# Performance work log

Hardware: AMD Instinct MI355X
Metric: run time of the kernel (lower is better)

Reference implementation:

```python
import jax, jax.numpy as jnp
import numpy as np

V, T_BLOCK, E, H, L = 65, 256, 384, 6, 10
HS = E // H  # 64


def _ln(x, scale, bias, eps=1e-5):
    mu = jnp.mean(x, axis=-1, keepdims=True)
    var = jnp.mean(jnp.square(x - mu), axis=-1, keepdims=True)
    return (x - mu) * jax.lax.rsqrt(var + eps) * scale + bias


def setup_inputs() -> dict:
    key = jax.random.key(0)
    ks = jax.random.split(key, 20)
    B, T = 64, 256
    s = 0.02
    return {
        "encoding": jax.random.randint(ks[0], (B, T), 0, V),
        "tok_emb": jax.random.normal(ks[1], (V, E), jnp.float32) * s,
        "pos_emb": jax.random.normal(ks[2], (T_BLOCK, E), jnp.float32) * s,
        "Wq": jax.random.normal(ks[3], (L, H, E, HS), jnp.float32) * s,
        "Wk": jax.random.normal(ks[4], (L, H, E, HS), jnp.float32) * s,
        "Wv": jax.random.normal(ks[5], (L, H, E, HS), jnp.float32) * s,
        "Wo": jax.random.normal(ks[6], (L, E, E), jnp.float32) * s,
        "bo": jnp.zeros((L, E), jnp.float32),
        "W1": jax.random.normal(ks[7], (L, E, 4 * E), jnp.float32) * s,
        "b1": jnp.zeros((L, 4 * E), jnp.float32),
        "W2": jax.random.normal(ks[8], (L, 4 * E, E), jnp.float32) * s,
        "b2": jnp.zeros((L, E), jnp.float32),
        "ln1_s": jnp.ones((L, E), jnp.float32),
        "ln1_b": jnp.zeros((L, E), jnp.float32),
        "ln2_s": jnp.ones((L, E), jnp.float32),
        "ln2_b": jnp.zeros((L, E), jnp.float32),
        "lnf_s": jnp.ones((E,), jnp.float32),
        "lnf_b": jnp.zeros((E,), jnp.float32),
        "Wout": jax.random.normal(ks[9], (E, V), jnp.float32) * s,
        "bout": jnp.zeros((V,), jnp.float32),
    }


def reference(encoding, tok_emb, pos_emb, Wq, Wk, Wv, Wo, bo, W1, b1, W2, b2,
              ln1_s, ln1_b, ln2_s, ln2_b, lnf_s, lnf_b, Wout, bout):
    B, T = encoding.shape
    x = tok_emb[encoding] + pos_emb[:T]  # [B,T,E]
    causal = jnp.tril(jnp.ones((T, T), bool))
    scale = jnp.asarray(E, x.dtype) ** -0.5  # NOTE: original scales by embeddingSize, not headSize
    for l in range(L):
        h = _ln(x, ln1_s[l], ln1_b[l])
        q = jnp.einsum('bte,hed->bhtd', h, Wq[l])
        k = jnp.einsum('bte,hed->bhtd', h, Wk[l])
        v = jnp.einsum('bte,hed->bhtd', h, Wv[l])
        scores = jnp.einsum('bhtd,bhsd->bhts', q, k) * scale
        scores = jnp.where(causal, scores, -jnp.inf)
        w = jax.nn.softmax(scores, axis=-1)  # dropout inactive (eval)
        attn = jnp.einsum('bhts,bhsd->bhtd', w, v)  # [B,H,T,HS]
        attn = attn.transpose(0, 2, 1, 3).reshape(B, T, E)  # concat heads
        x = x + attn @ Wo[l] + bo[l]
        h2 = _ln(x, ln2_s[l], ln2_b[l])
        x = x + jax.nn.relu(h2 @ W1[l] + b1[l]) @ W2[l] + b2[l]
    x = _ln(x, lnf_s, lnf_b)
    logits = x @ Wout + bout  # [B,T,V]
    return logits
```

## Files before the change

kernel.cpp:

```cpp
#include <hip/hip_runtime.h>

typedef __bf16 bf16;
typedef __bf16 bf16x4 __attribute__((ext_vector_type(4)));
typedef __bf16 bf16x8 __attribute__((ext_vector_type(8)));
typedef float floatx4 __attribute__((ext_vector_type(4)));

#define NB   64
#define NT   256
#define NE   384
#define NH   6
#define NHS  64
#define NL   10
#define NTOK (NB*NT)
#define NFF  1536
#define NQKV 1152
#define NV   65
#define NVP  128

#define ATTN_SCALE 0.051031036307982884f

__device__ __forceinline__ void glds16(const bf16* g, bf16* l)
{
    __builtin_amdgcn_global_load_lds(
        (const __attribute__((address_space(1))) void*)g,
        (__attribute__((address_space(3))) void*)l, 16, 0, 0);
}

template<int K, int N>
__global__ __launch_bounds__(256) void pack_mat_t(const float* __restrict__ src, bf16* __restrict__ dst)
{
    __shared__ float tile[64][65];
    const int n0 = blockIdx.x * 64, k0 = blockIdx.y * 64, l = blockIdx.z;
    const int tid = threadIdx.x;
    const float* sp = src + (size_t)l * K * N;
#pragma unroll
    for (int it = 0; it < 4; ++it) {
        int kl = (tid >> 4) + it * 16;
        int nl = (tid & 15) * 4;
        float4 v = *(const float4*)(sp + (size_t)(k0 + kl) * N + n0 + nl);
        tile[kl][nl] = v.x; tile[kl][nl + 1] = v.y; tile[kl][nl + 2] = v.z; tile[kl][nl + 3] = v.w;
    }
    __syncthreads();
#pragma unroll
    for (int it = 0; it < 2; ++it) {
        int chunk = it * 256 + tid;
        int nl = chunk >> 3, kc = chunk & 7;
        bf16x8 o;
#pragma unroll
        for (int j = 0; j < 8; ++j) o[j] = (bf16)tile[kc * 8 + j][nl];
        *(bf16x8*)(dst + ((size_t)l * N + n0 + nl) * K + k0 + kc * 8) = o;
    }
}

__global__ __launch_bounds__(256) void pack_qkv_t(const float* __restrict__ Wq, const float* __restrict__ Wk,
                                                  const float* __restrict__ Wv, bf16* __restrict__ dst)
{
    __shared__ float tile[64][65];
    const int n0 = blockIdx.x * 64, k0 = blockIdx.y * 64, l = blockIdx.z;
    const int tid = threadIdx.x;
    const float* src; int hh;
    if (n0 < 384)      { src = Wq; hh = n0 >> 6; }
    else if (n0 < 768) { src = Wk; hh = (n0 - 384) >> 6; }
    else               { src = Wv; hh = (n0 - 768) >> 6; }
    const float* sp = src + ((size_t)l * NH + hh) * NE * NHS;
#pragma unroll
    for (int it = 0; it < 4; ++it) {
        int kl = (tid >> 4) + it * 16;
        int dl = (tid & 15) * 4;
        float4 v = *(const float4*)(sp + (size_t)(k0 + kl) * NHS + dl);
        tile[kl][dl] = v.x; tile[kl][dl + 1] = v.y; tile[kl][dl + 2] = v.z; tile[kl][dl + 3] = v.w;
    }
    __syncthreads();
#pragma unroll
    for (int it = 0; it < 2; ++it) {
        int chunk = it * 256 + tid;
        int nl = chunk >> 3, kc = chunk & 7;
        bf16x8 o;
#pragma unroll
        for (int j = 0; j < 8; ++j) o[j] = (bf16)tile[kc * 8 + j][nl];
        *(bf16x8*)(dst + ((size_t)l * NQKV + n0 + nl) * NE + k0 + kc * 8) = o;
    }
}

__global__ void pack_wout_kernel(const float* __restrict__ Wout, const float* __restrict__ bout,
                                 bf16* __restrict__ dst, float* __restrict__ bias)
{
    int i = blockIdx.x * 256 + threadIdx.x;
    if (i >= NVP * NE) return;
    int k = i % NE, n = i / NE;
    dst[i] = (n < NV) ? (bf16)Wout[(size_t)k * NV + n] : (bf16)0.f;
    if (i < NVP) bias[i] = (i < NV) ? bout[i] : 0.f;
}

__global__ void embed_kernel(const int* __restrict__ enc, const float* __restrict__ tok,
                             const float* __restrict__ pos, bf16* __restrict__ x)
{
    int i = blockIdx.x * 256 + threadIdx.x;
    if (i >= NTOK * 96) return;
    int row = i / 96, e4 = i % 96;
    int t = row & (NT - 1);
    const float4* tp = (const float4*)(tok + (size_t)enc[row] * NE);
    const float4* pp = (const float4*)(pos + (size_t)t * NE);
    float4 a = tp[e4], p = pp[e4];
    bf16x4 r;
    r[0] = (bf16)(a.x + p.x); r[1] = (bf16)(a.y + p.y);
    r[2] = (bf16)(a.z + p.z); r[3] = (bf16)(a.w + p.w);
    *(bf16x4*)(x + (size_t)row * NE + e4 * 4) = r;
}

__global__ __launch_bounds__(256) void ln_kernel(const bf16* __restrict__ xin,
                                                 const float* __restrict__ gam,
                                                 const float* __restrict__ bet,
                                                 bf16* __restrict__ out)
{
    int wave = threadIdx.x >> 6, lane = threadIdx.x & 63;
    size_t row = (size_t)blockIdx.x * 4 + wave;
    const bf16x4* xr = (const bf16x4*)(xin + row * NE);
    bf16x4 c0 = xr[lane];
    bf16x4 c1 = (lane < 32) ? xr[64 + lane] : (bf16x4)(bf16)0.f;
    float v[8]; float sum = 0.f;
#pragma unroll
    for (int j = 0; j < 4; ++j) { v[j] = (float)c0[j]; sum += v[j]; }
#pragma unroll
    for (int j = 0; j < 4; ++j) { v[4 + j] = (float)c1[j]; sum += v[4 + j]; }
#pragma unroll
    for (int o = 1; o < 64; o <<= 1) sum += __shfl_xor(sum, o);
    float mu = sum * (1.f / NE);
    float var = 0.f;
#pragma unroll
    for (int j = 0; j < 4; ++j) { float d = v[j] - mu; var += d * d; }
    if (lane < 32) {
#pragma unroll
        for (int j = 0; j < 4; ++j) { float d = v[4 + j] - mu; var += d * d; }
    }
#pragma unroll
    for (int o = 1; o < 64; o <<= 1) var += __shfl_xor(var, o);
    float rs = rsqrtf(var * (1.f / NE) + 1e-5f);
    bf16x4* orow = (bf16x4*)(out + row * NE);
    {
        float4 g = ((const float4*)gam)[lane], bb = ((const float4*)bet)[lane];
        bf16x4 o4;
        o4[0] = (bf16)((v[0] - mu) * rs * g.x + bb.x);
        o4[1] = (bf16)((v[1] - mu) * rs * g.y + bb.y);
        o4[2] = (bf16)((v[2] - mu) * rs * g.z + bb.z);
        o4[3] = (bf16)((v[3] - mu) * rs * g.w + bb.w);
        orow[lane] = o4;
    }
    if (lane < 32) {
        float4 g = ((const float4*)gam)[64 + lane], bb = ((const float4*)bet)[64 + lane];
        bf16x4 o4;
        o4[0] = (bf16)((v[4] - mu) * rs * g.x + bb.x);
        o4[1] = (bf16)((v[5] - mu) * rs * g.y + bb.y);
        o4[2] = (bf16)((v[6] - mu) * rs * g.z + bb.z);
        o4[3] = (bf16)((v[7] - mu) * rs * g.w + bb.w);
        orow[64 + lane] = o4;
    }
}

template<int MT, bool BIAS, bool RELU, bool RESID, bool OUTBF16, bool VSPLIT>
__global__ __launch_bounds__(256, 4)
void gemm_kernel(const bf16* __restrict__ A, const bf16* __restrict__ Bt,
                 const float* __restrict__ bias, const bf16* __restrict__ resid,
                 void* __restrict__ outp, bf16* __restrict__ vt,
                 int M, int K, int out_stride, int n_store)
{
    constexpr int MI = MT / 32;
    __shared__ bf16 As[MT * 64];
    __shared__ bf16 Bs[128 * 64];
    const int tid  = threadIdx.x;
    const int wave = tid >> 6;
    const int lane = tid & 63;
    const int quad = lane >> 4;
    const int l16  = lane & 15;
    const int lrow = lane >> 3;
    const int scol = ((lane & 7) ^ lrow) * 8;
    const int m0 = blockIdx.x * MT;
    const int n0 = blockIdx.y * 128;
    const int wm = (wave >> 1) * (MT / 2);
    const int wn = (wave & 1) * 64;

    floatx4 acc[MI][4];
#pragma unroll
    for (int i = 0; i < MI; ++i)
#pragma unroll
        for (int j = 0; j < 4; ++j) acc[i][j] = (floatx4)0.f;

    const bf16* Ag = A  + (size_t)m0 * K;
    const bf16* Bg = Bt + (size_t)n0 * K;

    for (int k0 = 0; k0 < K; k0 += 64) {
#pragma unroll
        for (int it = 0; it < MT / 32; ++it) {
            int r0 = wave * (MT / 4) + it * 8;
            glds16(Ag + (size_t)(r0 + lrow) * K + k0 + scol, &As[r0 * 64]);
        }
#pragma unroll
        for (int it = 0; it < 4; ++it) {
            int r0 = wave * 32 + it * 8;
            glds16(Bg + (size_t)(r0 + lrow) * K + k0 + scol, &Bs[r0 * 64]);
        }
        __syncthreads();
#pragma unroll
        for (int ko = 0; ko < 2; ++ko) {
            bf16x8 af[MI], bfr[4];
#pragma unroll
            for (int mi = 0; mi < MI; ++mi) {
                int r = wm + mi * 16 + l16;
                int c = ((ko * 4 + quad) ^ (r & 7)) * 8;
                af[mi] = *(const bf16x8*)(&As[r * 64 + c]);
            }
#pragma unroll
            for (int ni = 0; ni < 4; ++ni) {
                int r = wn + ni * 16 + l16;
                int c = ((ko * 4 + quad) ^ (r & 7)) * 8;
                bfr[ni] = *(const bf16x8*)(&Bs[r * 64 + c]);
            }
#pragma unroll
            for (int mi = 0; mi < MI; ++mi)
#pragma unroll
                for (int ni = 0; ni < 4; ++ni)
                    acc[mi][ni] = __builtin_amdgcn_mfma_f32_16x16x32_bf16(af[mi], bfr[ni], acc[mi][ni], 0, 0, 0);
        }
        __syncthreads();
    }

#pragma unroll
    for (int mi = 0; mi < MI; ++mi) {
#pragma unroll
        for (int ni = 0; ni < 4; ++ni) {
            int n = n0 + wn + ni * 16 + l16;
            if (VSPLIT && n >= 768) {
                int nn = n - 768;
                int hh = nn >> 6, d = nn & 63;
                int mb = m0 + wm + mi * 16 + quad * 4;
                int bb = mb >> 8, tt = mb & 255;
                bf16x4 pv;
#pragma unroll
                for (int r = 0; r < 4; ++r) pv[r] = (bf16)acc[mi][ni][r];
                *(bf16x4*)(vt + ((size_t)(bb * NH + hh) * NHS + d) * NT + tt) = pv;
                continue;
            }
            float bv = 0.f;
            if (BIAS) bv = bias[n];
#pragma unroll
            for (int r = 0; r < 4; ++r) {
                int m = m0 + wm + mi * 16 + quad * 4 + r;
                float vv = acc[mi][ni][r] + bv;
                if (RELU) vv = fmaxf(vv, 0.f);
                if (n < n_store) {
                    size_t oi = (size_t)m * out_stride + n;
                    if (RESID) vv += (float)resid[oi];
                    if (OUTBF16) ((bf16*)outp)[oi] = (bf16)vv;
                    else         ((float*)outp)[oi] = vv;
                }
            }
        }
    }
}

__global__ __launch_bounds__(256, 3)
void attn_flash_kernel(const bf16* __restrict__ qkv, const bf16* __restrict__ vt,
                       bf16* __restrict__ outp)
{
    __shared__ bf16 Qs[128 * 64];
    __shared__ bf16 Ks[64 * 64];
    __shared__ bf16 Vs[64 * 64];
    __shared__ bf16 Ps[128 * 72];
    const int m0 = blockIdx.x * 128;
    const int z  = blockIdx.y;
    const int b = z / NH, hh = z % NH;
    const int tid = threadIdx.x;
    const int wave = tid >> 6, lane = tid & 63;
    const int quad = lane >> 4, l16 = lane & 15;
    const int lrow = lane >> 3;
    const int scol = ((lane & 7) ^ lrow) * 8;
    const int wm = wave * 32;
    const size_t qbase = (size_t)b * NT * NQKV + hh * NHS;
    const bf16* Vg = vt + (size_t)z * NHS * NT;

#pragma unroll
    for (int it = 0; it < 4; ++it) {
        int r0 = wave * 32 + it * 8;
        glds16(qkv + qbase + (size_t)(m0 + r0 + lrow) * NQKV + scol, &Qs[r0 * 64]);
    }

    floatx4 acc_o[2][4];
    float   psum[2][4];
#pragma unroll
    for (int mi = 0; mi < 2; ++mi) {
#pragma unroll
        for (int ni = 0; ni < 4; ++ni) acc_o[mi][ni] = (floatx4)0.f;
#pragma unroll
        for (int rr = 0; rr < 4; ++rr) psum[mi][rr] = 0.f;
    }

    const int n_ch = (m0 >> 6) + 2;
    for (int ch = 0; ch < n_ch; ++ch) {
        const int s0 = ch * 64;
        {
            int r0 = wave * 16;
            glds16(qkv + qbase + 384 + (size_t)(s0 + r0 + lrow) * NQKV + scol, &Ks[r0 * 64]);
            glds16(qkv + qbase + 384 + (size_t)(s0 + r0 + 8 + lrow) * NQKV + scol, &Ks[(r0 + 8) * 64]);
            glds16(Vg + (size_t)(r0 + lrow) * NT + s0 + scol, &Vs[r0 * 64]);
            glds16(Vg + (size_t)(r0 + 8 + lrow) * NT + s0 + scol, &Vs[(r0 + 8) * 64]);
        }
        __syncthreads();

        floatx4 accs[2][4];
#pragma unroll
        for (int mi = 0; mi < 2; ++mi)
#pragma unroll
            for (int ni = 0; ni < 4; ++ni) accs[mi][ni] = (floatx4)0.f;
#pragma unroll
        for (int ko = 0; ko < 2; ++ko) {
            bf16x8 af[2], bfr[4];
#pragma unroll
            for (int mi = 0; mi < 2; ++mi) {
                int r = wm + mi * 16 + l16;
                af[mi] = *(const bf16x8*)(&Qs[r * 64 + ((ko * 4 + quad) ^ (r & 7)) * 8]);
            }
#pragma unroll
            for (int ni = 0; ni < 4; ++ni) {
                int r = ni * 16 + l16;
                bfr[ni] = *(const bf16x8*)(&Ks[r * 64 + ((ko * 4 + quad) ^ (r & 7)) * 8]);
            }
#pragma unroll
            for (int mi = 0; mi < 2; ++mi)
#pragma unroll
                for (int ni = 0; ni < 4; ++ni)
                    accs[mi][ni] = __builtin_amdgcn_mfma_f32_16x16x32_bf16(af[mi], bfr[ni], accs[mi][ni], 0, 0, 0);
        }

#pragma unroll
        for (int mi = 0; mi < 2; ++mi) {
#pragma unroll
            for (int rr = 0; rr < 4; ++rr) {
                int t = m0 + wm + mi * 16 + quad * 4 + rr;
                float ps = 0.f;
#pragma unroll
                for (int ni = 0; ni < 4; ++ni) {
                    int s = s0 + ni * 16 + l16;
                    float p = (s <= t) ? __expf(accs[mi][ni][rr] * ATTN_SCALE) : 0.f;
                    ps += p;
                    Ps[(wm + mi * 16 + quad * 4 + rr) * 72 + ni * 16 + l16] = (bf16)p;
                }
                psum[mi][rr] += ps;
            }
        }

#pragma unroll
        for (int ko = 0; ko < 2; ++ko) {
            bf16x8 af[2], bfr[4];
#pragma unroll
            for (int mi = 0; mi < 2; ++mi)
                af[mi] = *(const bf16x8*)(&Ps[(wm + mi * 16 + l16) * 72 + ko * 32 + quad * 8]);
#pragma unroll
            for (int ni = 0; ni < 4; ++ni) {
                int r = ni * 16 + l16;
                bfr[ni] = *(const bf16x8*)(&Vs[r * 64 + ((ko * 4 + quad) ^ (r & 7)) * 8]);
            }
#pragma unroll
            for (int mi = 0; mi < 2; ++mi)
#pragma unroll
                for (int ni = 0; ni < 4; ++ni)
                    acc_o[mi][ni] = __builtin_amdgcn_mfma_f32_16x16x32_bf16(af[mi], bfr[ni], acc_o[mi][ni], 0, 0, 0);
        }
        __syncthreads();
    }

#pragma unroll
    for (int mi = 0; mi < 2; ++mi) {
#pragma unroll
        for (int rr = 0; rr < 4; ++rr) {
            float s = psum[mi][rr];
            s += __shfl_xor(s, 1); s += __shfl_xor(s, 2);
            s += __shfl_xor(s, 4); s += __shfl_xor(s, 8);
            psum[mi][rr] = 1.f / s;
        }
    }
#pragma unroll
    for (int mi = 0; mi < 2; ++mi) {
#pragma unroll
        for (int ni = 0; ni < 4; ++ni) {
            int e = hh * NHS + ni * 16 + l16;
#pragma unroll
            for (int rr = 0; rr < 4; ++rr) {
                int m = m0 + wm + mi * 16 + quad * 4 + rr;
                outp[((size_t)b * NT + m) * NE + e] = (bf16)(acc_o[mi][ni][rr] * psum[mi][rr]);
            }
        }
    }
}

extern "C" void kernel_launch(void* const* d_in, const int* in_sizes, int n_in,
                              void* d_out, int out_size, void* d_ws, size_t ws_size,
                              hipStream_t stream)
{
    const int*   enc  = (const int*)d_in[0];
    const float* tok  = (const float*)d_in[1];
    const float* pos  = (const float*)d_in[2];
    const float* Wq   = (const float*)d_in[3];
    const float* Wk   = (const float*)d_in[4];
    const float* Wv   = (const float*)d_in[5];
    const float* Wo   = (const float*)d_in[6];
    const float* bo   = (const float*)d_in[7];
    const float* W1   = (const float*)d_in[8];
    const float* b1   = (const float*)d_in[9];
    const float* W2   = (const float*)d_in[10];
    const float* b2   = (const float*)d_in[11];
    const float* ln1s = (const float*)d_in[12];
    const float* ln1b = (const float*)d_in[13];
    const float* ln2s = (const float*)d_in[14];
    const float* ln2b = (const float*)d_in[15];
    const float* lnfs = (const float*)d_in[16];
    const float* lnfb = (const float*)d_in[17];
    const float* Wout = (const float*)d_in[18];
    const float* bout = (const float*)d_in[19];

    char* ws = (char*)d_ws;
    bf16*  x      = (bf16*)(ws + 0);
    bf16*  h      = (bf16*)(ws + 12582912);
    bf16*  qkvu   = (bf16*)(ws + 25165824);
    bf16*  attn   = (bf16*)(ws + 75497472);
    bf16*  wqkv   = (bf16*)(ws + 88080384);
    bf16*  wo     = (bf16*)(ws + 96927744);
    bf16*  w1     = (bf16*)(ws + 99876864);
    bf16*  w2     = (bf16*)(ws + 111673344);
    bf16*  wop    = (bf16*)(ws + 123469824);
    float* bop    = (float*)(ws + 123568128);
    bf16*  vt     = (bf16*)(ws + 123568640);

    pack_qkv_t<<<dim3(18, 6, NL), 256, 0, stream>>>(Wq, Wk, Wv, wqkv);
    pack_mat_t<384, 384><<<dim3(6, 6, NL), 256, 0, stream>>>(Wo, wo);
    pack_mat_t<384, 1536><<<dim3(24, 6, NL), 256, 0, stream>>>(W1, w1);
    pack_mat_t<1536, 384><<<dim3(6, 24, NL), 256, 0, stream>>>(W2, w2);
    pack_wout_kernel<<<192, 256, 0, stream>>>(Wout, bout, wop, bop);
    embed_kernel<<<6144, 256, 0, stream>>>(enc, tok, pos, x);

    for (int l = 0; l < NL; ++l) {
        ln_kernel<<<4096, 256, 0, stream>>>(x, ln1s + l * NE, ln1b + l * NE, h);
        gemm_kernel<128, false, false, false, true, true><<<dim3(128, 9), 256, 0, stream>>>(
            h, wqkv + (size_t)l * NQKV * NE, nullptr, nullptr, qkvu, vt, NTOK, NE, NQKV, NQKV);
        attn_flash_kernel<<<dim3(2, NB * NH), 256, 0, stream>>>(qkvu, vt, attn);
        gemm_kernel<64, true, false, true, true, false><<<dim3(256, 3), 256, 0, stream>>>(
            attn, wo + (size_t)l * NE * NE, bo + l * NE, x, x, nullptr, NTOK, NE, NE, NE);
        ln_kernel<<<4096, 256, 0, stream>>>(x, ln2s + l * NE, ln2b + l * NE, h);
        gemm_kernel<128, true, true, false, true, false><<<dim3(128, 12), 256, 0, stream>>>(
            h, w1 + (size_t)l * NFF * NE, b1 + l * NFF, nullptr, qkvu, nullptr, NTOK, NE, NFF, NFF);
        gemm_kernel<64, true, false, true, true, false><<<dim3(256, 3), 256, 0, stream>>>(
            qkvu, w2 + (size_t)l * NE * NFF, b2 + l * NE, x, x, nullptr, NTOK, NFF, NE, NE);
    }
    ln_kernel<<<4096, 256, 0, stream>>>(x, lnfs, lnfb, h);
    gemm_kernel<64, true, false, false, false, false><<<dim3(256, 1), 256, 0, stream>>>(
        h, wop, bop, nullptr, d_out, nullptr, NTOK, NE, NV, NV);
}
```

Before: 1.417 ms.

## Fuse LayerNorm into residual GEMM epilogues and embedding kernel

New measurement: 1.620 ms. 14.3% more time.

```diff
diff --git a/kernel.cpp b/kernel.cpp
--- a/kernel.cpp
+++ b/kernel.cpp
@@ -92,37 +92,29 @@
     if (i < NVP) bias[i] = (i < NV) ? bout[i] : 0.f;
 }
 
-__global__ void embed_kernel(const int* __restrict__ enc, const float* __restrict__ tok,
-                             const float* __restrict__ pos, bf16* __restrict__ x)
-{
-    int i = blockIdx.x * 256 + threadIdx.x;
-    if (i >= NTOK * 96) return;
-    int row = i / 96, e4 = i % 96;
-    int t = row & (NT - 1);
+__global__ __launch_bounds__(256) void embed_ln_kernel(const int* __restrict__ enc,
+                                                       const float* __restrict__ tok,
+                                                       const float* __restrict__ pos,
+                                                       const float* __restrict__ gam,
+                                                       const float* __restrict__ bet,
+                                                       bf16* __restrict__ x, bf16* __restrict__ h)
+{
+    int wave = threadIdx.x >> 6, lane = threadIdx.x & 63;
+    size_t row = (size_t)blockIdx.x * 4 + wave;
+    int t = (int)(row & (NT - 1));
     const float4* tp = (const float4*)(tok + (size_t)enc[row] * NE);
     const float4* pp = (const float4*)(pos + (size_t)t * NE);
-    float4 a = tp[e4], p = pp[e4];
-    bf16x4 r;
-    r[0] = (bf16)(a.x + p.x); r[1] = (bf16)(a.y + p.y);
-    r[2] = (bf16)(a.z + p.z); r[3] = (bf16)(a.w + p.w);
-    *(bf16x4*)(x + (size_t)row * NE + e4 * 4) = r;
-}
-
-__global__ __launch_bounds__(256) void ln_kernel(const bf16* __restrict__ xin,
-                                                 const float* __restrict__ gam,
-                                                 const float* __restrict__ bet,
-                                                 bf16* __restrict__ out)
-{
-    int wave = threadIdx.x >> 6, lane = threadIdx.x & 63;
-    size_t row = (size_t)blockIdx.x * 4 + wave;
-    const bf16x4* xr = (const bf16x4*)(xin + row * NE);
-    bf16x4 c0 = xr[lane];
-    bf16x4 c1 = (lane < 32) ? xr[64 + lane] : (bf16x4)(bf16)0.f;
     float v[8]; float sum = 0.f;
-#pragma unroll
-    for (int j = 0; j < 4; ++j) { v[j] = (float)c0[j]; sum += v[j]; }
-#pragma unroll
-    for (int j = 0; j < 4; ++j) { v[4 + j] = (float)c1[j]; sum += v[4 + j]; }
+    {
+        float4 a = tp[lane], p = pp[lane];
+        v[0] = a.x + p.x; v[1] = a.y + p.y; v[2] = a.z + p.z; v[3] = a.w + p.w;
+        sum = v[0] + v[1] + v[2] + v[3];
+    }
+    if (lane < 32) {
+        float4 a = tp[64 + lane], p = pp[64 + lane];
+        v[4] = a.x + p.x; v[5] = a.y + p.y; v[6] = a.z + p.z; v[7] = a.w + p.w;
+        sum += v[4] + v[5] + v[6] + v[7];
+    } else { v[4] = v[5] = v[6] = v[7] = 0.f; }
 #pragma unroll
     for (int o = 1; o < 64; o <<= 1) sum += __shfl_xor(sum, o);
     float mu = sum * (1.f / NE);
@@ -136,24 +128,27 @@
 #pragma unroll
     for (int o = 1; o < 64; o <<= 1) var += __shfl_xor(var, o);
     float rs = rsqrtf(var * (1.f / NE) + 1e-5f);
-    bf16x4* orow = (bf16x4*)(out + row * NE);
+    bf16x4* xrow = (bf16x4*)(x + row * NE);
+    bf16x4* hrow = (bf16x4*)(h + row * NE);
     {
         float4 g = ((const float4*)gam)[lane], bb = ((const float4*)bet)[lane];
-        bf16x4 o4;
-        o4[0] = (bf16)((v[0] - mu) * rs * g.x + bb.x);
-        o4[1] = (bf16)((v[1] - mu) * rs * g.y + bb.y);
-        o4[2] = (bf16)((v[2] - mu) * rs * g.z + bb.z);
-        o4[3] = (bf16)((v[3] - mu) * rs * g.w + bb.w);
-        orow[lane] = o4;
+        bf16x4 xo, ho;
+        xo[0] = (bf16)v[0]; xo[1] = (bf16)v[1]; xo[2] = (bf16)v[2]; xo[3] = (bf16)v[3];
+        ho[0] = (bf16)((v[0] - mu) * rs * g.x + bb.x);
+        ho[1] = (bf16)((v[1] - mu) * rs * g.y + bb.y);
+        ho[2] = (bf16)((v[2] - mu) * rs * g.z + bb.z);
+        ho[3] = (bf16)((v[3] - mu) * rs * g.w + bb.w);
+        xrow[lane] = xo; hrow[lane] = ho;
     }
     if (lane < 32) {
         float4 g = ((const float4*)gam)[64 + lane], bb = ((const float4*)bet)[64 + lane];
-        bf16x4 o4;
-        o4[0] = (bf16)((v[4] - mu) * rs * g.x + bb.x);
-        o4[1] = (bf16)((v[5] - mu) * rs * g.y + bb.y);
-        o4[2] = (bf16)((v[6] - mu) * rs * g.z + bb.z);
-        o4[3] = (bf16)((v[7] - mu) * rs * g.w + bb.w);
-        orow[64 + lane] = o4;
+        bf16x4 xo, ho;
+        xo[0] = (bf16)v[4]; xo[1] = (bf16)v[5]; xo[2] = (bf16)v[6]; xo[3] = (bf16)v[7];
+        ho[0] = (bf16)((v[4] - mu) * rs * g.x + bb.x);
+        ho[1] = (bf16)((v[5] - mu) * rs * g.y + bb.y);
+        ho[2] = (bf16)((v[6] - mu) * rs * g.z + bb.z);
+        ho[3] = (bf16)((v[7] - mu) * rs * g.w + bb.w);
+        xrow[64 + lane] = xo; hrow[64 + lane] = ho;
     }
 }
 
@@ -253,6 +248,112 @@
                     if (OUTBF16) ((bf16*)outp)[oi] = (bf16)vv;
                     else         ((float*)outp)[oi] = vv;
                 }
+            }
+        }
+    }
+}
+
+__global__ __launch_bounds__(256, 2)
+void gemm_resid_ln_kernel(const bf16* __restrict__ A, const bf16* __restrict__ Bt,
+                          const float* __restrict__ bias,
+                          bf16* __restrict__ x, bf16* __restrict__ hout,
+                          const float* __restrict__ gam, const float* __restrict__ bet,
+                          int K)
+{
+    __shared__ bf16 As[64 * 64];
+    __shared__ bf16 Bs[384 * 64];
+    __shared__ float ssum[4][64], ssq[4][64];
+    const int tid  = threadIdx.x;
+    const int wave = tid >> 6;
+    const int lane = tid & 63;
+    const int quad = lane >> 4;
+    const int l16  = lane & 15;
+    const int lrow = lane >> 3;
+    const int scol = ((lane & 7) ^ lrow) * 8;
+    const int m0 = blockIdx.x * 64;
+    const int wn = wave * 96;
+
+    floatx4 acc[4][6];
+#pragma unroll
+    for (int i = 0; i < 4; ++i)
+#pragma unroll
+        for (int j = 0; j < 6; ++j) acc[i][j] = (floatx4)0.f;
+
+    const bf16* Ag = A + (size_t)m0 * K;
+
+    for (int k0 = 0; k0 < K; k0 += 64) {
+        glds16(Ag + (size_t)(wave * 16 + lrow) * K + k0 + scol, &As[(wave * 16) * 64]);
+        glds16(Ag + (size_t)(wave * 16 + 8 + lrow) * K + k0 + scol, &As[(wave * 16 + 8) * 64]);
+#pragma unroll
+        for (int it = 0; it < 12; ++it) {
+            int r0 = wave * 96 + it * 8;
+            glds16(Bt + (size_t)(r0 + lrow) * K + k0 + scol, &Bs[r0 * 64]);
+        }
+        __syncthreads();
+#pragma unroll
+        for (int ko = 0; ko < 2; ++ko) {
+            bf16x8 af[4], bfr[6];
+#pragma unroll
+            for (int mi = 0; mi < 4; ++mi) {
+                int r = mi * 16 + l16;
+                af[mi] = *(const bf16x8*)(&As[r * 64 + ((ko * 4 + quad) ^ (r & 7)) * 8]);
+            }
+#pragma unroll
+            for (int ni = 0; ni < 6; ++ni) {
+                int r = wn + ni * 16 + l16;
+                bfr[ni] = *(const bf16x8*)(&Bs[r * 64 + ((ko * 4 + quad) ^ (r & 7)) * 8]);
+            }
+#pragma unroll
+            for (int mi = 0; mi < 4; ++mi)
+#pragma unroll
+                for (int ni = 0; ni < 6; ++ni)
+                    acc[mi][ni] = __builtin_amdgcn_mfma_f32_16x16x32_bf16(af[mi], bfr[ni], acc[mi][ni], 0, 0, 0);
+        }
+        __syncthreads();
+    }
+
+    float bv[6], gv[6], bb[6];
+#pragma unroll
+    for (int ni = 0; ni < 6; ++ni) {
+        int n = wn + ni * 16 + l16;
+        bv[ni] = bias[n]; gv[ni] = gam[n]; bb[ni] = bet[n];
+    }
+#pragma unroll
+    for (int mi = 0; mi < 4; ++mi) {
+#pragma unroll
+        for (int rr = 0; rr < 4; ++rr) {
+            int rl = mi * 16 + quad * 4 + rr;
+            bf16* xrow = x + (size_t)(m0 + rl) * NE;
+            float s = 0.f, q = 0.f;
+#pragma unroll
+            for (int ni = 0; ni < 6; ++ni) {
+                int n = wn + ni * 16 + l16;
+                float vv = acc[mi][ni][rr] + bv[ni] + (float)xrow[n];
+                acc[mi][ni][rr] = vv;
+                xrow[n] = (bf16)vv;
+                s += vv; q += vv * vv;
+            }
+            s += __shfl_xor(s, 1); s += __shfl_xor(s, 2); s += __shfl_xor(s, 4); s += __shfl_xor(s, 8);
+            q += __shfl_xor(q, 1); q += __shfl_xor(q, 2); q += __shfl_xor(q, 4); q += __shfl_xor(q, 8);
+            if (l16 == 0) { ssum[wave][rl] = s; ssq[wave][rl] = q; }
+        }
+    }
+    __syncthreads();
+#pragma unroll
+    for (int mi = 0; mi < 4; ++mi) {
+#pragma unroll
+        for (int rr = 0; rr < 4; ++rr) {
+            int rl = mi * 16 + quad * 4 + rr;
+            float sum = ssum[0][rl] + ssum[1][rl] + ssum[2][rl] + ssum[3][rl];
+            float sq  = ssq[0][rl]  + ssq[1][rl]  + ssq[2][rl]  + ssq[3][rl];
+            float mu = sum * (1.f / NE);
+            float var = sq * (1.f / NE) - mu * mu;
+            float rs = rsqrtf(var + 1e-5f);
+            bf16* hrow = hout + (size_t)(m0 + rl) * NE;
+#pragma unroll
+            for (int ni = 0; ni < 6; ++ni) {
+                int n = wn + ni * 16 + l16;
+                hrow[n] = (bf16)((acc[mi][ni][rr] - mu) * rs * gv[ni] + bb[ni]);
             }
         }
     }
@@ -435,22 +536,22 @@
     pack_mat_t<384, 1536><<<dim3(24, 6, NL), 256, 0, stream>>>(W1, w1);
     pack_mat_t<1536, 384><<<dim3(6, 24, NL), 256, 0, stream>>>(W2, w2);
     pack_wout_kernel<<<192, 256, 0, stream>>>(Wout, bout, wop, bop);
-    embed_kernel<<<6144, 256, 0, stream>>>(enc, tok, pos, x);
+    embed_ln_kernel<<<4096, 256, 0, stream>>>(enc, tok, pos, ln1s, ln1b, x, h);
 
     for (int l = 0; l < NL; ++l) {
-        ln_kernel<<<4096, 256, 0, stream>>>(x, ln1s + l * NE, ln1b + l * NE, h);
         gemm_kernel<128, false, false, false, true, true><<<dim3(128, 9), 256, 0, stream>>>(
             h, wqkv + (size_t)l * NQKV * NE, nullptr, nullptr, qkvu, vt, NTOK, NE, NQKV, NQKV);
         attn_flash_kernel<<<dim3(2, NB * NH), 256, 0, stream>>>(qkvu, vt, attn);
-        gemm_kernel<64, true, false, true, true, false><<<dim3(256, 3), 256, 0, stream>>>(
-            attn, wo + (size_t)l * NE * NE, bo + l * NE, x, x, nullptr, NTOK, NE, NE, NE);
-        ln_kernel<<<4096, 256, 0, stream>>>(x, ln2s + l * NE, ln2b + l * NE, h);
+        gemm_resid_ln_kernel<<<256, 256, 0, stream>>>(
+            attn, wo + (size_t)l * NE * NE, bo + l * NE, x, h,
+            ln2s + l * NE, ln2b + l * NE, NE);
         gemm_kernel<128, true, true, false, true, false><<<dim3(128, 12), 256, 0, stream>>>(
             h, w1 + (size_t)l * NFF * NE, b1 + l * NFF, nullptr, qkvu, nullptr, NTOK, NE, NFF, NFF);
-        gemm_kernel<64, true, false, true, true, false><<<dim3(256, 3), 256, 0, stream>>>(
-            qkvu, w2 + (size_t)l * NE * NFF, b2 + l * NE, x, x, nullptr, NTOK, NFF, NE, NE);
-    }
-    ln_kernel<<<4096, 256, 0, stream>>>(x, lnfs, lnfb, h);
+        const float* ng = (l < NL - 1) ? (ln1s + (l + 1) * NE) : lnfs;
+        const float* nb = (l < NL - 1) ? (ln1b + (l + 1) * NE) : lnfb;
+        gemm_resid_ln_kernel<<<256, 256, 0, stream>>>(
+            qkvu, w2 + (size_t)l * NE * NFF, b2 + l * NE, x, h, ng, nb, NFF);
+    }
     gemm_kernel<64, true, false, false, false, false><<<dim3(256, 1), 256, 0, stream>>>(
         h, wop, bop, nullptr, d_out, nullptr, NTOK, NE, NV, NV);
 }
```
